# Performance work log

Measured on AMD Instinct MI355X. Metric: run time of the kernel, lower is better.

## Reference

```python
import jax, jax.numpy as jnp
import numpy as np


@jax.custom_vjp
def spike(mem, v_th):
    # Heaviside forward, triangular surrogate backward (gamma=1.0)
    return (mem >= v_th).astype(mem.dtype)


def _spike_fwd(mem, v_th):
    return spike(mem, v_th), (mem, v_th)


def _spike_bwd(res, g):
    mem, v_th = res
    surr = jnp.clip(1.0 - jnp.abs(mem - v_th), 0.0)  # gamma = 1
    return (g * surr, jnp.zeros_like(v_th))  # torch returns None for threshold grad


spike.defvjp(_spike_fwd, _spike_bwd)


def setup_inputs() -> dict:
    key = jax.random.key(0)
    ks = jax.random.split(key, 6)
    T, B, C, H, W = 8, 16, 256, 32, 32
    NH, HID = 4, 64
    x = jax.random.normal(ks[0], (T, B, C, H, W), dtype=jnp.float32)
    decay_param = jnp.float32(np.log(0.85 / 0.15))  # logit(0.85)
    v_th = jnp.float32(0.5)
    W1 = jax.random.normal(ks[1], (NH, HID, T), dtype=jnp.float32) * 0.1
    b1 = jax.random.normal(ks[2], (NH, HID), dtype=jnp.float32) * 0.01
    W2 = jax.random.normal(ks[3], (NH, T, HID), dtype=jnp.float32) * 0.1
    b2 = jax.random.normal(ks[4], (NH, T), dtype=jnp.float32) * 0.01
    att_w = jnp.ones((NH,), dtype=jnp.float32) / NH
    return {"x": x, "decay_param": decay_param, "v_th": v_th,
            "W1": W1, "b1": b1, "W2": W2, "b2": b2, "att_w": att_w}


def reference(x, decay_param, v_th, W1, b1, W2, b2, att_w):
    T, B, C, H, W = x.shape
    d = jax.nn.sigmoid(decay_param)

    def step(carry, inp):
        mem, spk = carry  # detached states, as in the torch module
        m = d * (mem - v_th * spk) + inp
        denom = jnp.mean(jnp.abs(m), axis=(1, 2, 3), keepdims=True) + 1e-6
        m = m / denom
        s = spike(m, v_th)
        carry = (jax.lax.stop_gradient(m), jax.lax.stop_gradient(s))
        return carry, s

    init = (jnp.zeros_like(x[0]), jnp.zeros_like(x[0]))
    _, spikes = jax.lax.scan(step, init, x)          # [T,B,C,H,W]

    feats = spikes.reshape(T, B, C * H * W)          # [T,B,F]
    summary = feats.mean(axis=2).T                   # [B,T]
    # multi-head MLP attention over time
    h = jax.nn.relu(jnp.einsum('bt,nht->bnh', summary, W1) + b1[None])  # [B,NH,HID]
    maps = jnp.einsum('bnh,nth->bnt', h, W2) + b2[None]                  # [B,NH,T]
    weighted = jnp.sum(maps * att_w[None, :, None], axis=1)              # [B,T]
    aw = jax.nn.softmax(weighted, axis=-1).T[:, :, None]                 # [T,B,1]
    out = jnp.sum(feats * aw, axis=0)                                    # [B,F]
    return out
```

## Files before the change

kernel.cpp:

```cpp
#include <hip/hip_runtime.h>

#define NT    8
#define NB    16
#define FS    262144
#define TPB   512
#define NW    8
#define BPB   16
#define GRID  (NB*BPB)
#define CHK   8
#define ELB   (TPB*CHK*4)
#define SPIN_CAP (1L<<26)

#define K_BIAS  67108864.0
#define TGT_D   1073741824.0
#define B_BIAS  524288
#define TGT_I   8388608

#define WS_NEED 16384

__device__ __forceinline__ void bar_lds() {
    __builtin_amdgcn_sched_barrier(0);
    asm volatile("s_waitcnt lgkmcnt(0)" ::: "memory");
    __builtin_amdgcn_s_barrier();
    __builtin_amdgcn_sched_barrier(0);
}

__global__ __launch_bounds__(TPB, 2)
void bispike_kernel(const float* __restrict__ x,
                    const float* __restrict__ decay_p,
                    const float* __restrict__ vth_p,
                    const float* __restrict__ W1,
                    const float* __restrict__ b1,
                    const float* __restrict__ W2,
                    const float* __restrict__ b2,
                    const float* __restrict__ att_w,
                    float* __restrict__ out,
                    char* __restrict__ wsb)
{
    const int tid  = threadIdx.x;
    const int lane = tid & 63;
    const int wid  = tid >> 6;
    const int b    = blockIdx.x & 15;
    const int bg   = blockIdx.x >> 4;

    const double dec  = 1.0 / (1.0 + exp(-(double)decay_p[0]));
    const double vth  = (double)vth_p[0];
    const double csub = dec * vth;

    double   u[CHK * 4];
    float4   xv[CHK];
    unsigned sm[NT];

    {
        const float* p = x + (size_t)b * FS + (size_t)bg * ELB + tid * 4;
        #pragma unroll
        for (int k = 0; k < CHK; ++k) xv[k] = *(const float4*)(p + k * (TPB * 4));
    }
    double lsum;
    {
        double n0 = 0.0, n1 = 0.0, n2 = 0.0, n3 = 0.0;
        #pragma unroll
        for (int k = 0; k < CHK; ++k) {
            u[k*4+0] = (double)xv[k].x; n0 += fabs(u[k*4+0]);
            u[k*4+1] = (double)xv[k].y; n1 += fabs(u[k*4+1]);
            u[k*4+2] = (double)xv[k].z; n2 += fabs(u[k*4+2]);
            u[k*4+3] = (double)xv[k].w; n3 += fabs(u[k*4+3]);
        }
        lsum = (n0 + n1) + (n2 + n3);
    }

    __shared__ double dred[NW];
    __shared__ double denom_s;

    #pragma unroll 1
    for (int t = 0; t < NT; ++t) {
        if (t < NT - 1) {
            const float* p = x + ((size_t)(t + 1) * NB + b) * FS
                               + (size_t)bg * ELB + tid * 4;
            #pragma unroll
            for (int k = 0; k < CHK; ++k) xv[k] = *(const float4*)(p + k * (TPB * 4));
        }

        double ls = lsum;
        #pragma unroll
        for (int off = 32; off > 0; off >>= 1)
            ls += __shfl_down(ls, off, 64);
        if (lane == 0) dred[wid] = ls;
        bar_lds();

        if (wid == 0) {
            if (lane == 0) {
                const double bs = (((dred[0] + dred[1]) + (dred[2] + dred[3]))
                                 + ((dred[4] + dred[5]) + (dred[6] + dred[7])));
                double* acc = (double*)(wsb + (size_t)(t * NB + b) * 64);
                double ret = __hip_atomic_fetch_add(acc, bs + K_BIAS,
                                 __ATOMIC_RELAXED, __HIP_MEMORY_SCOPE_AGENT);
                double v = ret + (bs + K_BIAS);
                if (v < TGT_D - 1.0) {
                    long it = 0;
                    for (;;) {
                        v = __hip_atomic_load(acc, __ATOMIC_RELAXED,
                                              __HIP_MEMORY_SCOPE_AGENT);
                        if (v >= TGT_D - 1.0) break;
                        if (++it > SPIN_CAP) break;
                        __builtin_amdgcn_s_sleep(2);
                    }
                }
                denom_s = (v - TGT_D) / (double)FS + 1e-6;
            }
        }
        bar_lds();
        const double denom = denom_s;

        const double thr = vth * denom;
        const double a   = dec * (1.0 / denom);
        unsigned smt = 0;
        if (t < NT - 1) {
            double n0 = 0.0, n1 = 0.0, n2 = 0.0, n3 = 0.0;
            #pragma unroll
            for (int k = 0; k < CHK; ++k) {
                const double xn0 = (double)xv[k].x, xn1 = (double)xv[k].y,
                             xn2 = (double)xv[k].z, xn3 = (double)xv[k].w;
                double un;
                bool s0 = (u[k*4+0] >= thr); if (s0) smt |= 1u << (k*4+0);
                un = fma(a, u[k*4+0], xn0); if (s0) un -= csub;
                u[k*4+0] = un; n0 += fabs(un);
                bool s1 = (u[k*4+1] >= thr); if (s1) smt |= 1u << (k*4+1);
                un = fma(a, u[k*4+1], xn1); if (s1) un -= csub;
                u[k*4+1] = un; n1 += fabs(un);
                bool s2 = (u[k*4+2] >= thr); if (s2) smt |= 1u << (k*4+2);
                un = fma(a, u[k*4+2], xn2); if (s2) un -= csub;
                u[k*4+2] = un; n2 += fabs(un);
                bool s3 = (u[k*4+3] >= thr); if (s3) smt |= 1u << (k*4+3);
                un = fma(a, u[k*4+3], xn3); if (s3) un -= csub;
                u[k*4+3] = un; n3 += fabs(un);
            }
            lsum = (n0 + n1) + (n2 + n3);
        } else {
            #pragma unroll
            for (int j = 0; j < CHK * 4; ++j)
                if (u[j] >= thr) smt |= 1u << j;
        }
        sm[t] = smt;
    }

    __shared__ int ired[NT][NW];
    #pragma unroll
    for (int t = 0; t < NT; ++t) {
        int c = __popc(sm[t]);
        #pragma unroll
        for (int off = 32; off > 0; off >>= 1)
            c += __shfl_down(c, off, 64);
        if (lane == 0) ired[t][wid] = c;
    }
    __syncthreads();

    __shared__ int totc_s[NT];
    __shared__ double summ_s[NT];

    if (wid == 0) {
        int* cp = (int*)(wsb + 8192 + (size_t)(lane * NB + b) * 64);
        int v = TGT_I;
        if (lane < NT) {
            int tot = 0;
            #pragma unroll
            for (int w = 0; w < NW; ++w) tot += ired[lane][w];
            int ret = __hip_atomic_fetch_add(cp, tot + B_BIAS,
                          __ATOMIC_RELAXED, __HIP_MEMORY_SCOPE_AGENT);
            v = ret + tot + B_BIAS;
        }
        long it = 0;
        while (!__all(v >= TGT_I)) {
            if (lane < NT && v < TGT_I)
                v = __hip_atomic_load(cp, __ATOMIC_RELAXED,
                                      __HIP_MEMORY_SCOPE_AGENT);
            if (++it > SPIN_CAP) break;
            __builtin_amdgcn_s_sleep(2);
        }
        if (lane < NT) totc_s[lane] = v - TGT_I;
    }
    __syncthreads();
    if (tid < NT)
        summ_s[tid] = (double)totc_s[tid] / (double)FS;
    __syncthreads();

    __shared__ double h_s[4 * 64];
    __shared__ double wmat_s[NT];
    if (tid < 256) {
        int nh = tid >> 6, hd = tid & 63;
        double acc = 0.0;
        #pragma unroll
        for (int t = 0; t < NT; ++t)
            acc += summ_s[t] * (double)W1[nh * 512 + hd * 8 + t];
        acc += (double)b1[nh * 64 + hd];
        h_s[tid] = fmax(acc, 0.0);
    }
    __syncthreads();
    if (tid < NT) {
        double w = 0.0;
        for (int nh = 0; nh < 4; ++nh) {
            double macc = 0.0;
            for (int hd = 0; hd < 64; ++hd)
                macc += h_s[nh * 64 + hd] * (double)W2[nh * 512 + tid * 64 + hd];
            macc += (double)b2[nh * 8 + tid];
            w += macc * (double)att_w[nh];
        }
        wmat_s[tid] = w;
    }
    __syncthreads();

    double awr[NT];
    {
        double mx = wmat_s[0];
        #pragma unroll
        for (int t = 1; t < NT; ++t) mx = fmax(mx, wmat_s[t]);
        double ss = 0.0;
        #pragma unroll
        for (int t = 0; t < NT; ++t) { awr[t] = exp(wmat_s[t] - mx); ss += awr[t]; }
        #pragma unroll
        for (int t = 0; t < NT; ++t) awr[t] = awr[t] / ss;
    }

    float* po = out + (size_t)b * FS + (size_t)bg * ELB + tid * 4;
    #pragma unroll
    for (int k = 0; k < CHK; ++k) {
        double o[4] = {0.0, 0.0, 0.0, 0.0};
        #pragma unroll
        for (int t = 0; t < NT; ++t) {
            const unsigned smt = sm[t];
            o[0] += ((smt >> (k * 4 + 0)) & 1) ? awr[t] : 0.0;
            o[1] += ((smt >> (k * 4 + 1)) & 1) ? awr[t] : 0.0;
            o[2] += ((smt >> (k * 4 + 2)) & 1) ? awr[t] : 0.0;
            o[3] += ((smt >> (k * 4 + 3)) & 1) ? awr[t] : 0.0;
        }
        *(float4*)(po + k * (TPB * 4)) =
            make_float4((float)o[0], (float)o[1], (float)o[2], (float)o[3]);
    }
}

__global__ void diag_kernel(float* out, int code) {
    out[0] = 100000.0f + (float)code;
}

extern "C" void kernel_launch(void* const* d_in, const int* in_sizes, int n_in,
                              void* d_out, int out_size, void* d_ws, size_t ws_size,
                              hipStream_t stream) {
    const float* x     = (const float*)d_in[0];
    const float* decay = (const float*)d_in[1];
    const float* vth   = (const float*)d_in[2];
    const float* W1    = (const float*)d_in[3];
    const float* b1    = (const float*)d_in[4];
    const float* W2    = (const float*)d_in[5];
    const float* b2    = (const float*)d_in[6];
    const float* att   = (const float*)d_in[7];
    float* out = (float*)d_out;

    if (ws_size < WS_NEED) {
        diag_kernel<<<1, 1, 0, stream>>>(out, 999);
        return;
    }

    hipMemsetAsync(d_ws, 0, WS_NEED, stream);

    hipGetLastError();
    bispike_kernel<<<dim3(GRID), dim3(TPB), 0, stream>>>(
        x, decay, vth, W1, b1, W2, b2, att, out, (char*)d_ws);
    hipError_t err = hipGetLastError();
    if (err != hipSuccess) {
        diag_kernel<<<1, 1, 0, stream>>>(out, (int)err);
    }
}
```

Before: 228.0 us.

## Add dedicated proxy wavefront for cross-block atomics and overlap spike-count publishing

Adds a ninth wavefront per block that only does the cross-block denominator atomic and spin-wait, so compute waves no longer run the serial reduction themselves. Per-timestep spike counts are reduced inside the loop and published by the proxy wave one step later, which overlaps the count atomics with the time scan. The cost is an extra idle wavefront per block and a dropped occupancy hint in launch bounds, which can change register allocation.

```diff
diff --git a/kernel.cpp b/kernel.cpp
--- a/kernel.cpp
+++ b/kernel.cpp
@@ -3,12 +3,13 @@
 #define NT    8
 #define NB    16
 #define FS    262144
-#define TPB   512
+#define DTPB  512
+#define TPB   576
 #define NW    8
 #define BPB   16
 #define GRID  (NB*BPB)
 #define CHK   8
-#define ELB   (TPB*CHK*4)
+#define ELB   (DTPB*CHK*4)
 #define SPIN_CAP (1L<<26)
 
 #define K_BIAS  67108864.0
@@ -25,7 +26,7 @@
     __builtin_amdgcn_sched_barrier(0);
 }
 
-__global__ __launch_bounds__(TPB, 2)
+__global__ __launch_bounds__(TPB)
 void bispike_kernel(const float* __restrict__ x,
                     const float* __restrict__ decay_p,
                     const float* __restrict__ vth_p,
@@ -40,6 +41,7 @@
     const int tid  = threadIdx.x;
     const int lane = tid & 63;
     const int wid  = tid >> 6;
+    const bool pw  = (wid == NW);
     const int b    = blockIdx.x & 15;
     const int bg   = blockIdx.x >> 4;
 
@@ -50,14 +52,13 @@
     double   u[CHK * 4];
     float4   xv[CHK];
     unsigned sm[NT];
-
-    {
+    int      csave = 0;
+
+    double lsum = 0.0;
+    if (!pw) {
         const float* p = x + (size_t)b * FS + (size_t)bg * ELB + tid * 4;
         #pragma unroll
-        for (int k = 0; k < CHK; ++k) xv[k] = *(const float4*)(p + k * (TPB * 4));
-    }
-    double lsum;
-    {
+        for (int k = 0; k < CHK; ++k) xv[k] = *(const float4*)(p + k * (DTPB * 4));
         double n0 = 0.0, n1 = 0.0, n2 = 0.0, n3 = 0.0;
         #pragma unroll
         for (int k = 0; k < CHK; ++k) {
@@ -71,104 +72,118 @@
 
     __shared__ double dred[NW];
     __shared__ double denom_s;
+    __shared__ int    ired[NT][NW];
 
     #pragma unroll 1
     for (int t = 0; t < NT; ++t) {
-        if (t < NT - 1) {
-            const float* p = x + ((size_t)(t + 1) * NB + b) * FS
-                               + (size_t)bg * ELB + tid * 4;
-            #pragma unroll
-            for (int k = 0; k < CHK; ++k) xv[k] = *(const float4*)(p + k * (TPB * 4));
-        }
-
-        double ls = lsum;
-        #pragma unroll
-        for (int off = 32; off > 0; off >>= 1)
-            ls += __shfl_down(ls, off, 64);
-        if (lane == 0) dred[wid] = ls;
+        if (!pw) {
+            if (t < NT - 1) {
+                const float* p = x + ((size_t)(t + 1) * NB + b) * FS
+                                   + (size_t)bg * ELB + tid * 4;
+                #pragma unroll
+                for (int k = 0; k < CHK; ++k)
+                    xv[k] = *(const float4*)(p + k * (DTPB * 4));
+            }
+            double ls = lsum;
+            #pragma unroll
+            for (int off = 32; off > 0; off >>= 1)
+                ls += __shfl_down(ls, off, 64);
+            if (lane == 0) {
+                dred[wid] = ls;
+                if (t > 0) ired[t - 1][wid] = csave;
+            }
+        }
         bar_lds();
 
-        if (wid == 0) {
-            if (lane == 0) {
-                const double bs = (((dred[0] + dred[1]) + (dred[2] + dred[3]))
-                                 + ((dred[4] + dred[5]) + (dred[6] + dred[7])));
-                double* acc = (double*)(wsb + (size_t)(t * NB + b) * 64);
-                double ret = __hip_atomic_fetch_add(acc, bs + K_BIAS,
-                                 __ATOMIC_RELAXED, __HIP_MEMORY_SCOPE_AGENT);
-                double v = ret + (bs + K_BIAS);
-                if (v < TGT_D - 1.0) {
-                    long it = 0;
-                    for (;;) {
-                        v = __hip_atomic_load(acc, __ATOMIC_RELAXED,
-                                              __HIP_MEMORY_SCOPE_AGENT);
-                        if (v >= TGT_D - 1.0) break;
-                        if (++it > SPIN_CAP) break;
-                        __builtin_amdgcn_s_sleep(2);
-                    }
+        if (pw && lane == 0) {
+            double bs = 0.0;
+            #pragma unroll
+            for (int w = 0; w < NW; ++w) bs += dred[w];
+            double* acc = (double*)(wsb + (size_t)(t * NB + b) * 64);
+            double ret = __hip_atomic_fetch_add(acc, bs + K_BIAS,
+                             __ATOMIC_RELAXED, __HIP_MEMORY_SCOPE_AGENT);
+            double v = ret + (bs + K_BIAS);
+            if (v < TGT_D - 1.0) {
+                long it = 0;
+                for (;;) {
+                    v = __hip_atomic_load(acc, __ATOMIC_RELAXED,
+                                          __HIP_MEMORY_SCOPE_AGENT);
+                    if (v >= TGT_D - 1.0) break;
+                    if (++it > SPIN_CAP) break;
+                    __builtin_amdgcn_s_sleep(2);
                 }
-                denom_s = (v - TGT_D) / (double)FS + 1e-6;
-            }
+            }
+            denom_s = (v - TGT_D) / (double)FS + 1e-6;
         }
         bar_lds();
         const double denom = denom_s;
 
-        const double thr = vth * denom;
-        const double a   = dec * (1.0 / denom);
-        unsigned smt = 0;
-        if (t < NT - 1) {
-            double n0 = 0.0, n1 = 0.0, n2 = 0.0, n3 = 0.0;
-            #pragma unroll
-            for (int k = 0; k < CHK; ++k) {
-                const double xn0 = (double)xv[k].x, xn1 = (double)xv[k].y,
-                             xn2 = (double)xv[k].z, xn3 = (double)xv[k].w;
-                double un;
-                bool s0 = (u[k*4+0] >= thr); if (s0) smt |= 1u << (k*4+0);
-                un = fma(a, u[k*4+0], xn0); if (s0) un -= csub;
-                u[k*4+0] = un; n0 += fabs(un);
-                bool s1 = (u[k*4+1] >= thr); if (s1) smt |= 1u << (k*4+1);
-                un = fma(a, u[k*4+1], xn1); if (s1) un -= csub;
-                u[k*4+1] = un; n1 += fabs(un);
-                bool s2 = (u[k*4+2] >= thr); if (s2) smt |= 1u << (k*4+2);
-                un = fma(a, u[k*4+2], xn2); if (s2) un -= csub;
-                u[k*4+2] = un; n2 += fabs(un);
-                bool s3 = (u[k*4+3] >= thr); if (s3) smt |= 1u << (k*4+3);
-                un = fma(a, u[k*4+3], xn3); if (s3) un -= csub;
-                u[k*4+3] = un; n3 += fabs(un);
-            }
-            lsum = (n0 + n1) + (n2 + n3);
-        } else {
-            #pragma unroll
-            for (int j = 0; j < CHK * 4; ++j)
-                if (u[j] >= thr) smt |= 1u << j;
-        }
-        sm[t] = smt;
-    }
-
-    __shared__ int ired[NT][NW];
-    #pragma unroll
-    for (int t = 0; t < NT; ++t) {
-        int c = __popc(sm[t]);
-        #pragma unroll
-        for (int off = 32; off > 0; off >>= 1)
-            c += __shfl_down(c, off, 64);
-        if (lane == 0) ired[t][wid] = c;
-    }
+        if (!pw) {
+            const double thr = vth * denom;
+            const double a   = dec * (1.0 / denom);
+            unsigned smt = 0;
+            if (t < NT - 1) {
+                double n0 = 0.0, n1 = 0.0, n2 = 0.0, n3 = 0.0;
+                #pragma unroll
+                for (int k = 0; k < CHK; ++k) {
+                    const double xn0 = (double)xv[k].x, xn1 = (double)xv[k].y,
+                                 xn2 = (double)xv[k].z, xn3 = (double)xv[k].w;
+                    double un;
+                    bool s0 = (u[k*4+0] >= thr); if (s0) smt |= 1u << (k*4+0);
+                    un = fma(a, u[k*4+0], xn0); if (s0) un -= csub;
+                    u[k*4+0] = un; n0 += fabs(un);
+                    bool s1 = (u[k*4+1] >= thr); if (s1) smt |= 1u << (k*4+1);
+                    un = fma(a, u[k*4+1], xn1); if (s1) un -= csub;
+                    u[k*4+1] = un; n1 += fabs(un);
+                    bool s2 = (u[k*4+2] >= thr); if (s2) smt |= 1u << (k*4+2);
+                    un = fma(a, u[k*4+2], xn2); if (s2) un -= csub;
+                    u[k*4+2] = un; n2 += fabs(un);
+                    bool s3 = (u[k*4+3] >= thr); if (s3) smt |= 1u << (k*4+3);
+                    un = fma(a, u[k*4+3], xn3); if (s3) un -= csub;
+                    u[k*4+3] = un; n3 += fabs(un);
+                }
+                lsum = (n0 + n1) + (n2 + n3);
+            } else {
+                #pragma unroll
+                for (int j = 0; j < CHK * 4; ++j)
+                    if (u[j] >= thr) smt |= 1u << j;
+            }
+            sm[t] = smt;
+            int c = __popc(smt);
+            #pragma unroll
+            for (int off = 32; off > 0; off >>= 1)
+                c += __shfl_down(c, off, 64);
+            csave = c;
+        } else if (lane == 0 && t > 0) {
+            int tot = 0;
+            #pragma unroll
+            for (int w = 0; w < NW; ++w) tot += ired[t - 1][w];
+            (void)__hip_atomic_fetch_add(
+                (int*)(wsb + 8192 + (size_t)((t - 1) * NB + b) * 64),
+                tot + B_BIAS, __ATOMIC_RELAXED, __HIP_MEMORY_SCOPE_AGENT);
+        }
+    }
+
+    if (!pw && lane == 0) ired[NT - 1][wid] = csave;
     __syncthreads();
 
     __shared__ int totc_s[NT];
     __shared__ double summ_s[NT];
 
-    if (wid == 0) {
+    if (pw) {
+        if (lane == 0) {
+            int tot = 0;
+            #pragma unroll
+            for (int w = 0; w < NW; ++w) tot += ired[NT - 1][w];
+            (void)__hip_atomic_fetch_add(
+                (int*)(wsb + 8192 + (size_t)((NT - 1) * NB + b) * 64),
+                tot + B_BIAS, __ATOMIC_RELAXED, __HIP_MEMORY_SCOPE_AGENT);
+        }
         int* cp = (int*)(wsb + 8192 + (size_t)(lane * NB + b) * 64);
         int v = TGT_I;
-        if (lane < NT) {
-            int tot = 0;
-            #pragma unroll
-            for (int w = 0; w < NW; ++w) tot += ired[lane][w];
-            int ret = __hip_atomic_fetch_add(cp, tot + B_BIAS,
-                          __ATOMIC_RELAXED, __HIP_MEMORY_SCOPE_AGENT);
-            v = ret + tot + B_BIAS;
-        }
+        if (lane < NT)
+            v = __hip_atomic_load(cp, __ATOMIC_RELAXED,
+                                  __HIP_MEMORY_SCOPE_AGENT);
         long it = 0;
         while (!__all(v >= TGT_I)) {
             if (lane < NT && v < TGT_I)
@@ -221,20 +236,22 @@
         for (int t = 0; t < NT; ++t) awr[t] = awr[t] / ss;
     }
 
-    float* po = out + (size_t)b * FS + (size_t)bg * ELB + tid * 4;
-    #pragma unroll
-    for (int k = 0; k < CHK; ++k) {
-        double o[4] = {0.0, 0.0, 0.0, 0.0};
-        #pragma unroll
-        for (int t = 0; t < NT; ++t) {
-            const unsigned smt = sm[t];
-            o[0] += ((smt >> (k * 4 + 0)) & 1) ? awr[t] : 0.0;
-            o[1] += ((smt >> (k * 4 + 1)) & 1) ? awr[t] : 0.0;
-            o[2] += ((smt >> (k * 4 + 2)) & 1) ? awr[t] : 0.0;
-            o[3] += ((smt >> (k * 4 + 3)) & 1) ? awr[t] : 0.0;
-        }
-        *(float4*)(po + k * (TPB * 4)) =
-            make_float4((float)o[0], (float)o[1], (float)o[2], (float)o[3]);
+    if (!pw) {
+        float* po = out + (size_t)b * FS + (size_t)bg * ELB + tid * 4;
+        #pragma unroll
+        for (int k = 0; k < CHK; ++k) {
+            double o[4] = {0.0, 0.0, 0.0, 0.0};
+            #pragma unroll
+            for (int t = 0; t < NT; ++t) {
+                const unsigned smt = sm[t];
+                o[0] += ((smt >> (k * 4 + 0)) & 1) ? awr[t] : 0.0;
+                o[1] += ((smt >> (k * 4 + 1)) & 1) ? awr[t] : 0.0;
+                o[2] += ((smt >> (k * 4 + 2)) & 1) ? awr[t] : 0.0;
+                o[3] += ((smt >> (k * 4 + 3)) & 1) ? awr[t] : 0.0;
+            }
+            *(float4*)(po + k * (DTPB * 4)) =
+                make_float4((float)o[0], (float)o[1], (float)o[2], (float)o[3]);
+        }
     }
 }
 
```

Result: slower. 260.3 us (+14.2%).
